# Kernel optimization log

Measured on AMD Instinct MI355X. Metric: run time of the kernel, lower is better.

## Reference

```python
import jax, jax.numpy as jnp
import numpy as np

NEG = -1e30  # log-space 'zero' (avoids -inf NaN issues under jit)
EPS = 1e-7   # keras.backend.epsilon()


def _ctc_loss(y_true, y_pred):
    # y_true: [B, L] int labels in [0, C-1), y_pred: [B, T, C] softmax probs.
    # Keras ctc_batch_cost: logits = log(y_pred + eps), then tf.nn.ctc_loss
    # (which applies log_softmax internally), blank = C - 1.
    B, T, C = y_pred.shape
    L = y_true.shape[1]
    S = 2 * L + 1
    blank = C - 1

    logp = jax.nn.log_softmax(jnp.log(y_pred + EPS), axis=-1)  # [B, T, C]

    # Extended label sequence: blank, l1, blank, l2, ..., blank  -> [B, S]
    ext = jnp.full((B, S), blank, dtype=y_true.dtype).at[:, 1::2].set(y_true)
    lp_ext = jnp.take_along_axis(logp, ext[:, None, :].astype(jnp.int32), axis=2)  # [B, T, S]

    # skip transition s-2 -> s allowed iff ext[s] != blank and ext[s] != ext[s-2]
    ext_m2 = jnp.concatenate([jnp.full((B, 2), blank, ext.dtype), ext[:, :-2]], axis=1)
    allow_skip = (ext != blank) & (ext != ext_m2)
    allow_skip = allow_skip.at[:, :2].set(False)

    # alpha init at t=0
    alpha = jnp.full((B, S), NEG, dtype=logp.dtype)
    alpha = alpha.at[:, 0].set(lp_ext[:, 0, 0]).at[:, 1].set(lp_ext[:, 0, 1])

    neg1 = jnp.full((B, 1), NEG, dtype=logp.dtype)
    neg2 = jnp.full((B, 2), NEG, dtype=logp.dtype)

    def step(a, lp_t):
        prev1 = jnp.concatenate([neg1, a[:, :-1]], axis=1)
        prev2 = jnp.concatenate([neg2, a[:, :-2]], axis=1)
        acc = jnp.logaddexp(a, prev1)
        acc = jnp.where(allow_skip, jnp.logaddexp(acc, prev2), acc)
        return acc + lp_t, None

    lp_seq = jnp.transpose(lp_ext, (1, 0, 2))[1:]  # [T-1, B, S]
    alpha, _ = jax.lax.scan(step, alpha, lp_seq)

    loss = -jnp.logaddexp(alpha[:, -1], alpha[:, -2])  # [B]
    return loss[:, None]  # [B, 1] like keras ctc_batch_cost


def setup_inputs() -> dict:
    key = jax.random.key(0)
    k1, k2 = jax.random.split(key)
    B, T, C, L = 1024, 256, 128, 64
    y_true = jax.random.randint(k1, (B, L), 0, C - 1, dtype=jnp.int32)
    y_pred = jax.random.uniform(k2, (B, T, C), dtype=jnp.float32, minval=1e-4, maxval=1.0)
    return {"y_true": y_true, "y_pred": y_pred}


def reference(y_true, y_pred):
    return _ctc_loss(y_true, y_pred)
```

## Files before the change

### kernel.cpp

```cpp
#include <hip/hip_runtime.h>
#include <math.h>

#define BATCH 1024
#define TT    256
#define CC    128
#define LL    64
#define BLANK 127
#define EPSV  (1e-7f)

typedef _Float16 half_t;

template <int CTRL>
__device__ __forceinline__ float dpp0(float x) {
    return __int_as_float(__builtin_amdgcn_update_dpp(
        0, __float_as_int(x), CTRL, 0xF, 0xF, true));
}
template <int CTRL>
__device__ __forceinline__ float dppS(float x) {
    return __int_as_float(__builtin_amdgcn_update_dpp(
        __float_as_int(x), __float_as_int(x), CTRL, 0xF, 0xF, false));
}
__device__ __forceinline__ float wave_sum63(float s) {
    s += dpp0<0x111>(s);
    s += dpp0<0x112>(s);
    s += dpp0<0x114>(s);
    s += dpp0<0x118>(s);
    s += dpp0<0x142>(s);
    s += dpp0<0x143>(s);
    return s;
}
__device__ __forceinline__ float wave_max_bcast(float m) {
    m = fmaxf(m, dppS<0x111>(m));
    m = fmaxf(m, dppS<0x112>(m));
    m = fmaxf(m, dppS<0x114>(m));
    m = fmaxf(m, dppS<0x118>(m));
    m = fmaxf(m, dppS<0x142>(m));
    m = fmaxf(m, dppS<0x143>(m));
    return __int_as_float(__builtin_amdgcn_readlane(__float_as_int(m), 63));
}
__device__ __forceinline__ float rol1(float x) {
    return __int_as_float(__builtin_amdgcn_update_dpp(
        __float_as_int(x), __float_as_int(x), 0x134, 0xF, 0xF, false));
}

__global__ __launch_bounds__(256) void ctc_fwd_kernel(const int* __restrict__ y_true,
                                                      const float* __restrict__ y_pred,
                                                      float* __restrict__ out) {
    __shared__ half_t qtab[TT][66];
    __shared__ float  qblank[TT];
    __shared__ float  logZpart[4];
    __shared__ int    labels[LL];

    const int b    = blockIdx.x;
    const int tid  = threadIdx.x;
    const int wv   = tid >> 6;
    const int lane = tid & 63;

    const float* yp = y_pred + (size_t)b * (TT * CC);

    if (tid < LL) labels[tid] = y_true[b * LL + tid];
    __syncthreads();

    const int lab  = labels[lane];
    const int srcl = lab >> 1;

    float zacc = 0.0f;
    float2 v[8];
    #pragma unroll
    for (int j = 0; j < 8; ++j)
        v[j] = ((const float2*)(yp + (size_t)(wv + 4 * j) * CC))[lane];

    for (int k = 0; k < 8; ++k) {
        float2 vn[8];
        if (k < 7) {
            #pragma unroll
            for (int j = 0; j < 8; ++j)
                vn[j] = ((const float2*)(yp + (size_t)(wv + 32 * (k + 1) + 4 * j) * CC))[lane];
        }
        #pragma unroll
        for (int j = 0; j < 8; ++j) {
            const int t = wv + 32 * k + 4 * j;
            float q0 = v[j].x + EPSV, q1 = v[j].y + EPSV;
            float s = wave_sum63(q0 + q1);
            zacc += __logf(s);
            float ga = __shfl(q0, srcl);
            float gb = __shfl(q1, srcl);
            qtab[t][lane] = (half_t)((lab & 1) ? gb : ga);
            if (lane == 63) qblank[t] = q1;
        }
        #pragma unroll
        for (int j = 0; j < 8; ++j) v[j] = vn[j];
    }
    if (lane == 63) logZpart[wv] = zacc;
    __syncthreads();

    if (wv == 0) {
        const float logZ = logZpart[0] + logZpart[1] + logZpart[2] + logZpart[3];
        const int   labm1 = labels[(lane + 63) & 63];
        const float mskip = (lane >= 1 && lab != labm1) ? 1.0f : 0.0f;
        const bool  l0 = (lane == 0);

        float a0 = l0 ? qblank[0]            : 0.0f;
        float a1 = l0 ? (float)qtab[0][lane] : 0.0f;
        float aX = 0.0f;
        int Esum = 0;

        float qb = qblank[1];
        float ql = (float)qtab[1][lane];
        #pragma unroll 8
        for (int t = 1; t < TT; ++t) {
            float qb_n = 0.0f, ql_n = 0.0f;
            if (t + 1 < TT) { qb_n = qblank[t + 1]; ql_n = (float)qtab[t + 1][lane]; }
            float nb = rol1(a1);
            float nb0 = l0 ? 0.0f : nb;
            float na0 = (a0 + nb0) * qb;
            float na1 = fmaf(mskip, nb, a0 + a1) * ql;
            aX = l0 ? (aX + nb) * qb : 0.0f;
            a0 = na0; a1 = na1;
            if ((t & 7) == 7) {
                float m = fmaxf(a0, a1);
                m = fmaxf(m, l0 ? aX : 0.0f);
                float mall = wave_max_bcast(m);
                int ex = (int)((__float_as_uint(mall) >> 23) & 0xFF);
                int e  = 127 - ex;
                float sc = __uint_as_float((unsigned)(127 + e) << 23);
                a0 *= sc; a1 *= sc; aX *= sc;
                Esum += e;
            }
            qb = qb_n; ql = ql_n;
        }
        float a127 = __builtin_amdgcn_readlane(__float_as_int(a1), 63) != 0
                     ? __int_as_float(__builtin_amdgcn_readlane(__float_as_int(a1), 63))
                     : 0.0f;
        if (lane == 0) {
            float tot = aX + a127;
            out[b] = logZ + (float)Esum * 0.69314718055994531f - __logf(tot);
        }
    }
}

extern "C" void kernel_launch(void* const* d_in, const int* in_sizes, int n_in,
                              void* d_out, int out_size, void* d_ws, size_t ws_size,
                              hipStream_t stream) {
    const int*   y_true = (const int*)d_in[0];
    const float* y_pred = (const float*)d_in[1];
    float*       out    = (float*)d_out;
    ctc_fwd_kernel<<<BATCH, 256, 0, stream>>>(y_true, y_pred, out);
}
```

Measured before the change: 42.34 us.

## Use 512-thread blocks with float4 nontemporal loads covering two timesteps per wave

Doubles the block to 8 waves so more loaders stream the 128 KB of probabilities per batch row. Each lane now does a 16-byte nontemporal load covering two timesteps per wave instruction, with half-wave DPP reductions. Labels are gathered via packed fp16 shuffles, and the label array in shared memory is replaced by a register DPP rotate. The alpha recursion is restructured into explicit 8-step chunks with prefetched q values and unconditional renormalisation. This raises the register and occupancy demands of the block, and the single serial wave still leaves the other waves idle during the recursion.

```diff
diff --git a/kernel.cpp b/kernel.cpp
--- a/kernel.cpp
+++ b/kernel.cpp
@@ -5,29 +5,26 @@
 #define TT    256
 #define CC    128
 #define LL    64
-#define BLANK 127
 #define EPSV  (1e-7f)
 
-typedef _Float16 half_t;
+typedef float f32x4 __attribute__((ext_vector_type(4)));
 
 template <int CTRL>
 __device__ __forceinline__ float dpp0(float x) {
-    return __int_as_float(__builtin_amdgcn_update_dpp(
-        0, __float_as_int(x), CTRL, 0xF, 0xF, true));
+    return __int_as_float(__builtin_amdgcn_update_dpp(0, __float_as_int(x), CTRL, 0xF, 0xF, true));
 }
 template <int CTRL>
 __device__ __forceinline__ float dppS(float x) {
-    return __int_as_float(__builtin_amdgcn_update_dpp(
-        __float_as_int(x), __float_as_int(x), CTRL, 0xF, 0xF, false));
+    return __int_as_float(__builtin_amdgcn_update_dpp(__float_as_int(x), __float_as_int(x), CTRL, 0xF, 0xF, false));
 }
-__device__ __forceinline__ float wave_sum63(float s) {
-    s += dpp0<0x111>(s);
-    s += dpp0<0x112>(s);
-    s += dpp0<0x114>(s);
-    s += dpp0<0x118>(s);
-    s += dpp0<0x142>(s);
-    s += dpp0<0x143>(s);
-    return s;
+__device__ __forceinline__ float rol1_f(float x) {
+    return __int_as_float(__builtin_amdgcn_update_dpp(__float_as_int(x), __float_as_int(x), 0x134, 0xF, 0xF, false));
+}
+__device__ __forceinline__ int rol1_i(int x) {
+    return __builtin_amdgcn_update_dpp(x, x, 0x134, 0xF, 0xF, false);
+}
+__device__ __forceinline__ float rdlane(float x, int l) {
+    return __int_as_float(__builtin_amdgcn_readlane(__float_as_int(x), l));
 }
 __device__ __forceinline__ float wave_max_bcast(float m) {
     m = fmaxf(m, dppS<0x111>(m));
@@ -36,20 +33,24 @@
     m = fmaxf(m, dppS<0x118>(m));
     m = fmaxf(m, dppS<0x142>(m));
     m = fmaxf(m, dppS<0x143>(m));
-    return __int_as_float(__builtin_amdgcn_readlane(__float_as_int(m), 63));
+    return rdlane(m, 63);
 }
-__device__ __forceinline__ float rol1(float x) {
-    return __int_as_float(__builtin_amdgcn_update_dpp(
-        __float_as_int(x), __float_as_int(x), 0x134, 0xF, 0xF, false));
+__device__ __forceinline__ unsigned f2h(float x) {
+    _Float16 h = (_Float16)x;
+    unsigned short u; __builtin_memcpy(&u, &h, 2);
+    return (unsigned)u;
+}
+__device__ __forceinline__ float h2f(unsigned short u) {
+    _Float16 h; __builtin_memcpy(&h, &u, 2);
+    return (float)h;
 }
 
-__global__ __launch_bounds__(256) void ctc_fwd_kernel(const int* __restrict__ y_true,
-                                                      const float* __restrict__ y_pred,
-                                                      float* __restrict__ out) {
-    __shared__ half_t qtab[TT][66];
-    __shared__ float  qblank[TT];
-    __shared__ float  logZpart[4];
-    __shared__ int    labels[LL];
+__global__ __launch_bounds__(512, 8) void ctc_fwd_kernel(const int* __restrict__ y_true,
+                                                         const float* __restrict__ y_pred,
+                                                         float* __restrict__ out) {
+    __shared__ unsigned short qtab[TT][66];
+    __shared__ float qblank[TT];
+    __shared__ float logZpart[8];
 
     const int b    = blockIdx.x;
     const int tid  = threadIdx.x;
@@ -57,81 +58,116 @@
     const int lane = tid & 63;
 
     const float* yp = y_pred + (size_t)b * (TT * CC);
+    const int lab  = y_true[b * LL + lane];
+    const int srcA = lab >> 2;
+    const int srcB = 32 + srcA;
+    const bool hiPair = (lab & 2) != 0;
+    const bool hiHalf = (lab & 1) != 0;
 
-    if (tid < LL) labels[tid] = y_true[b * LL + tid];
-    __syncthreads();
-
-    const int lab  = labels[lane];
-    const int srcl = lab >> 1;
+    const int off = ((lane >> 5) << 7) + ((lane & 31) << 2);
+    const float* base = yp + off;
 
     float zacc = 0.0f;
-    float2 v[8];
+    f32x4 v[4];
     #pragma unroll
-    for (int j = 0; j < 8; ++j)
-        v[j] = ((const float2*)(yp + (size_t)(wv + 4 * j) * CC))[lane];
+    for (int j = 0; j < 4; ++j)
+        v[j] = __builtin_nontemporal_load((const f32x4*)(base + 256 * (wv + 8 * j)));
 
-    for (int k = 0; k < 8; ++k) {
-        float2 vn[8];
-        if (k < 7) {
+    for (int g = 0; g < 4; ++g) {
+        f32x4 vn[4];
+        if (g < 3) {
             #pragma unroll
-            for (int j = 0; j < 8; ++j)
-                vn[j] = ((const float2*)(yp + (size_t)(wv + 32 * (k + 1) + 4 * j) * CC))[lane];
+            for (int j = 0; j < 4; ++j)
+                vn[j] = __builtin_nontemporal_load((const f32x4*)(base + 256 * (wv + 32 * (g + 1) + 8 * j)));
         }
         #pragma unroll
-        for (int j = 0; j < 8; ++j) {
-            const int t = wv + 32 * k + 4 * j;
-            float q0 = v[j].x + EPSV, q1 = v[j].y + EPSV;
-            float s = wave_sum63(q0 + q1);
+        for (int j = 0; j < 4; ++j) {
+            const int r2 = wv + 32 * g + 8 * j;
+            const int tA = 2 * r2, tB = tA + 1;
+            float q0 = v[j][0] + EPSV, q1 = v[j][1] + EPSV;
+            float q2 = v[j][2] + EPSV, q3 = v[j][3] + EPSV;
+            float s = (q0 + q1) + (q2 + q3);
+            s += dpp0<0x111>(s);
+            s += dpp0<0x112>(s);
+            s += dpp0<0x114>(s);
+            s += dpp0<0x118>(s);
+            s += dpp0<0x142>(s);
             zacc += __logf(s);
-            float ga = __shfl(q0, srcl);
-            float gb = __shfl(q1, srcl);
-            qtab[t][lane] = (half_t)((lab & 1) ? gb : ga);
-            if (lane == 63) qblank[t] = q1;
+            int i01 = (int)(f2h(q0) | (f2h(q1) << 16));
+            int i23 = (int)(f2h(q2) | (f2h(q3) << 16));
+            int gA01 = __shfl(i01, srcA), gA23 = __shfl(i23, srcA);
+            int gB01 = __shfl(i01, srcB), gB23 = __shfl(i23, srcB);
+            int sA = hiPair ? gA23 : gA01;
+            int sB = hiPair ? gB23 : gB01;
+            qtab[tA][lane] = (unsigned short)(hiHalf ? ((unsigned)sA >> 16) : (sA & 0xFFFF));
+            qtab[tB][lane] = (unsigned short)(hiHalf ? ((unsigned)sB >> 16) : (sB & 0xFFFF));
+            if ((lane & 31) == 31) qblank[tA + (lane >> 5)] = q3;
         }
         #pragma unroll
-        for (int j = 0; j < 8; ++j) v[j] = vn[j];
+        for (int j = 0; j < 4; ++j) v[j] = vn[j];
     }
-    if (lane == 63) logZpart[wv] = zacc;
+    {
+        float z31 = rdlane(zacc, 31), z63 = rdlane(zacc, 63);
+        if (lane == 0) logZpart[wv] = z31 + z63;
+    }
     __syncthreads();
 
     if (wv == 0) {
-        const float logZ = logZpart[0] + logZpart[1] + logZpart[2] + logZpart[3];
-        const int   labm1 = labels[(lane + 63) & 63];
+        float logZ = 0.0f;
+        #pragma unroll
+        for (int w = 0; w < 8; ++w) logZ += logZpart[w];
+
+        const int labm1  = rol1_i(lab);
         const float mskip = (lane >= 1 && lab != labm1) ? 1.0f : 0.0f;
-        const bool  l0 = (lane == 0);
+        const bool l0 = (lane == 0);
 
-        float a0 = l0 ? qblank[0]            : 0.0f;
-        float a1 = l0 ? (float)qtab[0][lane] : 0.0f;
+        float a0 = l0 ? qblank[0] : 0.0f;
+        float a1 = l0 ? h2f(qtab[0][lane]) : 0.0f;
         float aX = 0.0f;
         int Esum = 0;
 
-        float qb = qblank[1];
-        float ql = (float)qtab[1][lane];
-        #pragma unroll 8
-        for (int t = 1; t < TT; ++t) {
-            float qb_n = 0.0f, ql_n = 0.0f;
-            if (t + 1 < TT) { qb_n = qblank[t + 1]; ql_n = (float)qtab[t + 1][lane]; }
-            float nb = rol1(a1);
-            float nb0 = l0 ? 0.0f : nb;
-            float na0 = (a0 + nb0) * qb;
-            float na1 = fmaf(mskip, nb, a0 + a1) * ql;
-            aX = l0 ? (aX + nb) * qb : 0.0f;
+        float qbv[8], qlv[8];
+        #pragma unroll
+        for (int i = 0; i < 8; ++i) {
+            qbv[i] = qblank[1 + i];
+            qlv[i] = h2f(qtab[1 + i][lane]);
+        }
+
+        for (int t0 = 1; t0 + 8 <= TT; t0 += 8) {
+            float qbn[8], qln[8];
+            #pragma unroll
+            for (int i = 0; i < 8; ++i) {
+                int tn = t0 + 8 + i; tn = (tn < TT) ? tn : (TT - 1);
+                qbn[i] = qblank[tn];
+                qln[i] = h2f(qtab[tn][lane]);
+            }
+            #pragma unroll
+            for (int i = 0; i < 8; ++i) {
+                float nb  = rol1_f(a1);
+                float na0 = (a0 + (l0 ? 0.0f : nb)) * qbv[i];
+                float na1 = fmaf(mskip, nb, a0 + a1) * qlv[i];
+                aX = l0 ? (aX + nb) * qbv[i] : 0.0f;
+                a0 = na0; a1 = na1;
+            }
+            float m = fmaxf(fmaxf(a0, a1), aX);
+            float mall = wave_max_bcast(m);
+            int ex = (int)((__float_as_uint(mall) >> 23) & 0xFF);
+            int e  = 127 - ex;
+            float sc = __uint_as_float((unsigned)(127 + e) << 23);
+            a0 *= sc; a1 *= sc; aX *= sc;
+            Esum += e;
+            #pragma unroll
+            for (int i = 0; i < 8; ++i) { qbv[i] = qbn[i]; qlv[i] = qln[i]; }
+        }
+        #pragma unroll
+        for (int i = 0; i < 7; ++i) {
+            float nb  = rol1_f(a1);
+            float na0 = (a0 + (l0 ? 0.0f : nb)) * qbv[i];
+            float na1 = fmaf(mskip, nb, a0 + a1) * qlv[i];
+            aX = l0 ? (aX + nb) * qbv[i] : 0.0f;
             a0 = na0; a1 = na1;
-            if ((t & 7) == 7) {
-                float m = fmaxf(a0, a1);
-                m = fmaxf(m, l0 ? aX : 0.0f);
-                float mall = wave_max_bcast(m);
-                int ex = (int)((__float_as_uint(mall) >> 23) & 0xFF);
-                int e  = 127 - ex;
-                float sc = __uint_as_float((unsigned)(127 + e) << 23);
-                a0 *= sc; a1 *= sc; aX *= sc;
-                Esum += e;
-            }
-            qb = qb_n; ql = ql_n;
         }
-        float a127 = __builtin_amdgcn_readlane(__float_as_int(a1), 63) != 0
-                     ? __int_as_float(__builtin_amdgcn_readlane(__float_as_int(a1), 63))
-                     : 0.0f;
+        float a127 = rdlane(a1, 63);
         if (lane == 0) {
             float tot = aX + a127;
             out[b] = logZ + (float)Esum * 0.69314718055994531f - __logf(tot);
@@ -145,5 +181,5 @@
     const int*   y_true = (const int*)d_in[0];
     const float* y_pred = (const float*)d_in[1];
     float*       out    = (float*)d_out;
-    ctc_fwd_kernel<<<BATCH, 256, 0, stream>>>(y_true, y_pred, out);
+    ctc_fwd_kernel<<<BATCH, 512, 0, stream>>>(y_true, y_pred, out);
 }
```

New measurement: 37.38 us. 1.13x faster.
